# Optimization experiments

Measured on AMD Instinct MI355X. Metric: run time of the kernel, lower is better.

Reference implementation:

```python
import jax, jax.numpy as jnp
import numpy as np

NOTE_RES = 64  # global constant in the original repo; equals D of rep


def _down(x):
    # conv1d with kernel [0.5, 0.5], stride 2 over last axis (even length)
    return 0.5 * (x[..., ::2] + x[..., 1::2])


def setup_inputs() -> dict:
    key = jax.random.key(0)
    k1, k2, k3 = jax.random.split(key, 3)
    B, D, T = 32, NOTE_RES, 4096
    rep = jax.random.normal(k1, (B, D, T), dtype=jnp.float32)
    duration_mask = jax.random.uniform(k2, (B, D, T), dtype=jnp.float32)
    position_mask = jax.random.uniform(k3, (B, D, T), dtype=jnp.float32)
    return {
        "rep": rep,
        "duration_mask": duration_mask,
        "position_mask": position_mask,
        "low_duration": 1,
        "up_duration": 64,
    }


def reference(rep, duration_mask, position_mask, low_duration, up_duration):
    B, D, T = rep.shape  # D == NOTE_RES
    x = jnp.transpose(rep, (0, 2, 1))  # [B, T, NOTE_RES]; conv axis is last
    densed = _down(x)                  # [B, T, NOTE_RES//2]
    pot = NOTE_RES // 2
    res = jnp.zeros((B, T), dtype=rep.dtype)
    for i in range(0, NOTE_RES - low_duration):
        win_len = NOTE_RES - i - 1
        if win_len == pot:
            # descend one pyramid level
            x = densed
            densed = _down(x) if i < NOTE_RES - 2 else None
            d = x  # [B, T, win_len]
            pot //= 2
        else:
            pad_len = win_len - pot
            # mix fine-resolution prefix with coarse suffix -> length win_len
            d = jnp.concatenate([x[..., : 2 * pad_len], densed[..., pad_len:]], axis=-1)
        if win_len < up_duration:
            # sum_w d[b,t,w] * position_mask[b,w,t], gated by duration_mask[b,win_len-1,t]
            contrib = duration_mask[:, win_len - 1, :] * jnp.einsum(
                "btw,bwt->bt", d, position_mask[:, :win_len, :]
            )
            res = res + contrib
    return res[:, None, :]  # [B, 1, T]
```

## Files before the change

### kernel.cpp

```cpp
#include <hip/hip_runtime.h>


#define TT 4096

template <int M>
__device__ __forceinline__ void group_accum(const float* __restrict__ dmb,
                                            const float* pmv, const float* xa,
                                            const float* q, int low, int up,
                                            float& res) {
#pragma unroll
  for (int pad = 0, _dummy = 0; pad < M; ++pad) {
    (void)_dummy;
  }
  float p = 0.f;
#pragma unroll
  for (int pad = 0; pad < M; ++pad) {
    const int L = M + pad;
    float s = p;
#pragma unroll
    for (int k = pad; k < M; ++k) s = fmaf(xa[k], pmv[k + pad], s);
    if (L >= low && L < up)
      res = fmaf(dmb[(size_t)(M - 1 + pad) * TT], s, res);
    p += q[pad];
  }
}

template <int M>
__device__ __forceinline__ void downsample(const float* pmv, float* xa,
                                           float* q) {
#pragma unroll
  for (int j = 0; j < M; ++j) {
    const float a = xa[2 * j];
    const float c = xa[2 * j + 1];
    q[j] = a * pmv[2 * j] + c * pmv[2 * j + 1];
    xa[j] = 0.5f * (a + c);
  }
}

__global__ __launch_bounds__(256, 2) void ContextGenerator_34875134444049_kernel(
    const float* __restrict__ rep, const float* __restrict__ dm,
    const float* __restrict__ pm, const int* __restrict__ lowp,
    const int* __restrict__ upp, float* __restrict__ out, int n) {
  const int gid = blockIdx.x * 256 + threadIdx.x;
  if (gid >= n) return;
  const int t = gid & (TT - 1);
  const int b = gid >> 12;
  const size_t base = (size_t)b * 64 * TT + (size_t)t;

  const int low = lowp[0];
  const int up = upp[0];

  const float* __restrict__ repb = rep + base;
  const float* __restrict__ dmb = dm + base;
  const float* __restrict__ pmb = pm + base;

  float pmv[63];
#pragma unroll
  for (int w = 0; w < 63; ++w) pmv[w] = pmb[(size_t)w * TT];

  float xa[32];
  float q[32];
#pragma unroll
  for (int j = 0; j < 32; ++j) {
    const float a = repb[(size_t)(2 * j) * TT];
    const float c = repb[(size_t)(2 * j + 1) * TT];
    xa[j] = 0.5f * (a + c);
    q[j] = a * pmv[2 * j] + c * pmv[2 * j + 1];
  }

  float res = 0.f;
  group_accum<32>(dmb, pmv, xa, q, low, up, res);
  downsample<16>(pmv, xa, q);
  group_accum<16>(dmb, pmv, xa, q, low, up, res);
  downsample<8>(pmv, xa, q);
  group_accum<8>(dmb, pmv, xa, q, low, up, res);
  downsample<4>(pmv, xa, q);
  group_accum<4>(dmb, pmv, xa, q, low, up, res);
  downsample<2>(pmv, xa, q);
  group_accum<2>(dmb, pmv, xa, q, low, up, res);
  downsample<1>(pmv, xa, q);
  group_accum<1>(dmb, pmv, xa, q, low, up, res);

  out[gid] = res;
}

extern "C" void kernel_launch(void* const* d_in, const int* in_sizes, int n_in,
                              void* d_out, int out_size, void* d_ws,
                              size_t ws_size, hipStream_t stream) {
  const float* rep = (const float*)d_in[0];
  const float* dm = (const float*)d_in[1];
  const float* pm = (const float*)d_in[2];
  const int* lowp = (const int*)d_in[3];
  const int* upp = (const int*)d_in[4];
  float* out = (float*)d_out;

  const int n = out_size;
  const int blocks = (n + 255) / 256;
  ContextGenerator_34875134444049_kernel<<<blocks, 256, 0, stream>>>(
      rep, dm, pm, lowp, upp, out, n);
}
```

Before: 143.1 us.

## Split per-column work across four waves with LDS staging of rep and pm

Each block now handles 64 time columns. Its four waves cooperatively stage the rep and position_mask tiles into shared memory using asynchronous global-to-LDS loads. The window work is split into unequal roles: three waves cover slices of the first pyramid level and one wave covers the lower levels, and the four partial sums are reduced through LDS. This is meant to cut the per-thread register footprint, allowing four blocks per CU instead of two and raising parallelism and latency hiding. The costs are block synchronisations, extra LDS traffic, and possible load imbalance between the roles.

```diff
diff --git a/kernel.cpp b/kernel.cpp
--- a/kernel.cpp
+++ b/kernel.cpp
@@ -3,85 +3,156 @@
 
 #define TT 4096
 
+__device__ __forceinline__ void async_load_f32(const float* g, float* l) {
+  __builtin_amdgcn_global_load_lds(
+      (const __attribute__((address_space(1))) void*)g,
+      (__attribute__((address_space(3))) void*)l, 4, 0, 0);
+}
+
+template <int P0, int P1>
+__device__ __forceinline__ float role32(const float* __restrict__ lrep,
+                                        const float* __restrict__ lpm,
+                                        const float* dmr, int lane, int low,
+                                        int up) {
+  float xa[32 - P0];
+#pragma unroll
+  for (int k = P0; k < 32; ++k)
+    xa[k - P0] = 0.5f * (lrep[(2 * k) * 64 + lane] + lrep[(2 * k + 1) * 64 + lane]);
+  float q[P1 - 1];
+#pragma unroll
+  for (int j = 0; j < P1 - 1; ++j)
+    q[j] = lrep[(2 * j) * 64 + lane] * lpm[(2 * j) * 64 + lane] +
+           lrep[(2 * j + 1) * 64 + lane] * lpm[(2 * j + 1) * 64 + lane];
+  float p = 0.f;
+#pragma unroll
+  for (int j = 0; j < P0; ++j) p += q[j];
+  float res = 0.f;
+#pragma unroll
+  for (int pad = P0; pad < P1; ++pad) {
+    const int L = 32 + pad;
+    float s = p;
+#pragma unroll
+    for (int k = pad; k < 32; ++k)
+      s = fmaf(xa[k - P0], lpm[(k + pad) * 64 + lane], s);
+    if (L >= low && L < up) res = fmaf(dmr[pad - P0], s, res);
+    if (pad + 1 < P1) p += q[pad];
+  }
+  return res;
+}
+
 template <int M>
-__device__ __forceinline__ void group_accum(const float* __restrict__ dmb,
-                                            const float* pmv, const float* xa,
-                                            const float* q, int low, int up,
-                                            float& res) {
+__device__ __forceinline__ void down_lds(const float* __restrict__ lpm, int lane,
+                                         float* xa, float* q) {
 #pragma unroll
-  for (int pad = 0, _dummy = 0; pad < M; ++pad) {
-    (void)_dummy;
+  for (int j = 0; j < M; ++j) {
+    const float a = xa[2 * j];
+    const float c = xa[2 * j + 1];
+    q[j] = a * lpm[(2 * j) * 64 + lane] + c * lpm[(2 * j + 1) * 64 + lane];
+    xa[j] = 0.5f * (a + c);
   }
+}
+
+template <int M>
+__device__ __forceinline__ void acc_lds(const float* __restrict__ lpm,
+                                        const float* dmr, int lane,
+                                        const float* xa, const float* q, int low,
+                                        int up, float& res) {
   float p = 0.f;
 #pragma unroll
   for (int pad = 0; pad < M; ++pad) {
     const int L = M + pad;
     float s = p;
 #pragma unroll
-    for (int k = pad; k < M; ++k) s = fmaf(xa[k], pmv[k + pad], s);
-    if (L >= low && L < up)
-      res = fmaf(dmb[(size_t)(M - 1 + pad) * TT], s, res);
+    for (int k = pad; k < M; ++k) s = fmaf(xa[k], lpm[(k + pad) * 64 + lane], s);
+    if (L >= low && L < up) res = fmaf(dmr[M - 1 + pad], s, res);
     p += q[pad];
   }
 }
 
-template <int M>
-__device__ __forceinline__ void downsample(const float* pmv, float* xa,
-                                           float* q) {
+__device__ __forceinline__ float role_tail(const float* __restrict__ lrep,
+                                           const float* __restrict__ lpm,
+                                           const float* dmr, int lane, int low,
+                                           int up) {
+  float xa[32];
 #pragma unroll
-  for (int j = 0; j < M; ++j) {
-    const float a = xa[2 * j];
-    const float c = xa[2 * j + 1];
-    q[j] = a * pmv[2 * j] + c * pmv[2 * j + 1];
-    xa[j] = 0.5f * (a + c);
-  }
+  for (int k = 0; k < 32; ++k)
+    xa[k] = 0.5f * (lrep[(2 * k) * 64 + lane] + lrep[(2 * k + 1) * 64 + lane]);
+  float q[16];
+  float res = 0.f;
+  down_lds<16>(lpm, lane, xa, q);
+  acc_lds<16>(lpm, dmr, lane, xa, q, low, up, res);
+  down_lds<8>(lpm, lane, xa, q);
+  acc_lds<8>(lpm, dmr, lane, xa, q, low, up, res);
+  down_lds<4>(lpm, lane, xa, q);
+  acc_lds<4>(lpm, dmr, lane, xa, q, low, up, res);
+  down_lds<2>(lpm, lane, xa, q);
+  acc_lds<2>(lpm, dmr, lane, xa, q, low, up, res);
+  down_lds<1>(lpm, lane, xa, q);
+  acc_lds<1>(lpm, dmr, lane, xa, q, low, up, res);
+  return res;
 }
 
-__global__ __launch_bounds__(256, 2) void ContextGenerator_34875134444049_kernel(
+__global__ __launch_bounds__(256, 4) void ContextGenerator_34875134444049_kernel(
     const float* __restrict__ rep, const float* __restrict__ dm,
     const float* __restrict__ pm, const int* __restrict__ lowp,
-    const int* __restrict__ upp, float* __restrict__ out, int n) {
-  const int gid = blockIdx.x * 256 + threadIdx.x;
-  if (gid >= n) return;
-  const int t = gid & (TT - 1);
-  const int b = gid >> 12;
-  const size_t base = (size_t)b * 64 * TT + (size_t)t;
+    const int* __restrict__ upp, float* __restrict__ out) {
+  __shared__ float lds[128 * 64 + 4 * 64];
+  const int wid = threadIdx.x >> 6;
+  const int lane = threadIdx.x & 63;
+  const int b = blockIdx.x >> 6;
+  const int t0 = (blockIdx.x & 63) << 6;
+
+  const size_t base = (size_t)b * 64 * TT + (size_t)t0;
+
+  for (int r = wid; r < 127; r += 4) {
+    const float* src = (r < 64) ? rep + base + (size_t)r * TT
+                                : pm + base + (size_t)(r - 64) * TT;
+    async_load_f32(src + lane, &lds[r * 64]);
+  }
 
   const int low = lowp[0];
   const int up = upp[0];
 
-  const float* __restrict__ repb = rep + base;
-  const float* __restrict__ dmb = dm + base;
-  const float* __restrict__ pmb = pm + base;
-
-  float pmv[63];
+  const float* dmb = dm + base + lane;
+  float dmr[31];
+  if (wid == 0) {
 #pragma unroll
-  for (int w = 0; w < 63; ++w) pmv[w] = pmb[(size_t)w * TT];
-
-  float xa[32];
-  float q[32];
+    for (int i = 0; i < 6; ++i) dmr[i] = dmb[(size_t)(31 + i) * TT];
+  } else if (wid == 1) {
 #pragma unroll
-  for (int j = 0; j < 32; ++j) {
-    const float a = repb[(size_t)(2 * j) * TT];
-    const float c = repb[(size_t)(2 * j + 1) * TT];
-    xa[j] = 0.5f * (a + c);
-    q[j] = a * pmv[2 * j] + c * pmv[2 * j + 1];
+    for (int i = 0; i < 7; ++i) dmr[i] = dmb[(size_t)(37 + i) * TT];
+  } else if (wid == 2) {
+#pragma unroll
+    for (int i = 0; i < 19; ++i) dmr[i] = dmb[(size_t)(44 + i) * TT];
+  } else {
+#pragma unroll
+    for (int i = 0; i < 31; ++i) dmr[i] = dmb[(size_t)i * TT];
   }
 
-  float res = 0.f;
-  group_accum<32>(dmb, pmv, xa, q, low, up, res);
-  downsample<16>(pmv, xa, q);
-  group_accum<16>(dmb, pmv, xa, q, low, up, res);
-  downsample<8>(pmv, xa, q);
-  group_accum<8>(dmb, pmv, xa, q, low, up, res);
-  downsample<4>(pmv, xa, q);
-  group_accum<4>(dmb, pmv, xa, q, low, up, res);
-  downsample<2>(pmv, xa, q);
-  group_accum<2>(dmb, pmv, xa, q, low, up, res);
-  downsample<1>(pmv, xa, q);
-  group_accum<1>(dmb, pmv, xa, q, low, up, res);
+  __syncthreads();
 
-  out[gid] = res;
+  const float* lrep = lds;
+  const float* lpm = lds + 64 * 64;
+
+  float res;
+  if (wid == 0)
+    res = role32<0, 6>(lrep, lpm, dmr, lane, low, up);
+  else if (wid == 1)
+    res = role32<6, 13>(lrep, lpm, dmr, lane, low, up);
+  else if (wid == 2)
+    res = role32<13, 32>(lrep, lpm, dmr, lane, low, up);
+  else
+    res = role_tail(lrep, lpm, dmr, lane, low, up);
+
+  float* part = lds + 128 * 64;
+  part[wid * 64 + lane] = res;
+  __syncthreads();
+
+  if (threadIdx.x < 64) {
+    const float r = part[threadIdx.x] + part[64 + threadIdx.x] +
+                    part[128 + threadIdx.x] + part[192 + threadIdx.x];
+    out[(size_t)b * TT + t0 + threadIdx.x] = r;
+  }
 }
 
 extern "C" void kernel_launch(void* const* d_in, const int* in_sizes, int n_in,
@@ -94,8 +165,7 @@
   const int* upp = (const int*)d_in[4];
   float* out = (float*)d_out;
 
-  const int n = out_size;
-  const int blocks = (n + 255) / 256;
+  const int blocks = out_size / 64;
   ContextGenerator_34875134444049_kernel<<<blocks, 256, 0, stream>>>(
-      rep, dm, pm, lowp, upp, out, n);
+      rep, dm, pm, lowp, upp, out);
 }
```

Result: faster. 125.9 us (-12.0%).

## Split per-timestep work across two wavefronts and reduce via shared memory

Applied to the files above, without the earlier changes.

Each output column is now handled by two wavefronts: one computes the finest pyramid level (window lengths 32..63) and the other computes the prefix-sum terms plus all coarser levels, and the two partial sums are combined through shared memory. This halves the serial per-thread work and register pressure, which is meant to raise parallelism and occupancy (launch bounds change to 128 threads, 4 blocks). The trade-off is duplicated reads of rep and position_mask by both wavefronts, an added block barrier, and the loss of the bounds check on out_size.

```diff
diff --git a/kernel.cpp b/kernel.cpp
--- a/kernel.cpp
+++ b/kernel.cpp
@@ -3,85 +3,140 @@
 
 #define TT 4096
 
-template <int M>
-__device__ __forceinline__ void group_accum(const float* __restrict__ dmb,
-                                            const float* pmv, const float* xa,
-                                            const float* q, int low, int up,
-                                            float& res) {
-#pragma unroll
-  for (int pad = 0, _dummy = 0; pad < M; ++pad) {
-    (void)_dummy;
-  }
-  float p = 0.f;
-#pragma unroll
-  for (int pad = 0; pad < M; ++pad) {
-    const int L = M + pad;
-    float s = p;
-#pragma unroll
-    for (int k = pad; k < M; ++k) s = fmaf(xa[k], pmv[k + pad], s);
-    if (L >= low && L < up)
-      res = fmaf(dmb[(size_t)(M - 1 + pad) * TT], s, res);
-    p += q[pad];
-  }
-}
-
-template <int M>
-__device__ __forceinline__ void downsample(const float* pmv, float* xa,
-                                           float* q) {
-#pragma unroll
-  for (int j = 0; j < M; ++j) {
-    const float a = xa[2 * j];
-    const float c = xa[2 * j + 1];
-    q[j] = a * pmv[2 * j] + c * pmv[2 * j + 1];
-    xa[j] = 0.5f * (a + c);
-  }
-}
-
-__global__ __launch_bounds__(256, 2) void ContextGenerator_34875134444049_kernel(
+__global__ __launch_bounds__(128, 4) void ContextGenerator_34875134444049_kernel(
     const float* __restrict__ rep, const float* __restrict__ dm,
     const float* __restrict__ pm, const int* __restrict__ lowp,
-    const int* __restrict__ upp, float* __restrict__ out, int n) {
-  const int gid = blockIdx.x * 256 + threadIdx.x;
-  if (gid >= n) return;
-  const int t = gid & (TT - 1);
-  const int b = gid >> 12;
-  const size_t base = (size_t)b * 64 * TT + (size_t)t;
+    const int* __restrict__ upp, float* __restrict__ out) {
+  __shared__ float part[64];
+  const int wid = threadIdx.x >> 6;
+  const int lane = threadIdx.x & 63;
+  const int b = blockIdx.x >> 6;
+  const int t0 = (blockIdx.x & 63) << 6;
+  const size_t base = (size_t)b * 64 * TT + (size_t)t0 + (size_t)lane;
 
+  const float* __restrict__ repc = rep + base;
+  const float* __restrict__ pmc = pm + base;
+  const float* __restrict__ dmc = dm + base;
   const int low = lowp[0];
   const int up = upp[0];
 
-  const float* __restrict__ repb = rep + base;
-  const float* __restrict__ dmb = dm + base;
-  const float* __restrict__ pmb = pm + base;
+  float res = 0.f;
 
-  float pmv[63];
+  if (wid == 0) {
+    float pmv[63];
 #pragma unroll
-  for (int w = 0; w < 63; ++w) pmv[w] = pmb[(size_t)w * TT];
+    for (int r = 0; r < 63; ++r) pmv[r] = pmc[(size_t)r * TT];
+    float x1[32];
+#pragma unroll
+    for (int j = 0; j < 32; ++j)
+      x1[j] = 0.5f * (repc[(size_t)(2 * j) * TT] + repc[(size_t)(2 * j + 1) * TT]);
+#pragma unroll
+    for (int pad = 0; pad < 32; ++pad) {
+      const int L = 32 + pad;
+      float s = 0.f;
+#pragma unroll
+      for (int k = pad; k < 32; ++k) s = fmaf(x1[k], pmv[k + pad], s);
+      if (L >= low && L < up) res = fmaf(dmc[(size_t)(31 + pad) * TT], s, res);
+    }
+  } else {
+    float x1[32], pmv[32];
+    float P = 0.f;
+#pragma unroll
+    for (int j = 0; j < 31; ++j) {
+      const float a = repc[(size_t)(2 * j) * TT];
+      const float c = repc[(size_t)(2 * j + 1) * TT];
+      const float pa = pmc[(size_t)(2 * j) * TT];
+      const float pc = pmc[(size_t)(2 * j + 1) * TT];
+      x1[j] = 0.5f * (a + c);
+      if (2 * j < 32) pmv[2 * j] = pa;
+      if (2 * j + 1 < 32) pmv[2 * j + 1] = pc;
+      P = fmaf(a, pa, fmaf(c, pc, P));
+      const int L = 33 + j;
+      if (L >= low && L < up) res = fmaf(dmc[(size_t)(32 + j) * TT], P, res);
+    }
+    x1[31] = 0.5f * (repc[(size_t)62 * TT] + repc[(size_t)63 * TT]);
 
-  float xa[32];
-  float q[32];
+    float x2[16], q1[16];
 #pragma unroll
-  for (int j = 0; j < 32; ++j) {
-    const float a = repb[(size_t)(2 * j) * TT];
-    const float c = repb[(size_t)(2 * j + 1) * TT];
-    xa[j] = 0.5f * (a + c);
-    q[j] = a * pmv[2 * j] + c * pmv[2 * j + 1];
+    for (int j = 0; j < 16; ++j) {
+      x2[j] = 0.5f * (x1[2 * j] + x1[2 * j + 1]);
+      q1[j] = fmaf(x1[2 * j], pmv[2 * j], x1[2 * j + 1] * pmv[2 * j + 1]);
+    }
+    float p = 0.f;
+#pragma unroll
+    for (int pad = 0; pad < 16; ++pad) {
+      const int L = 16 + pad;
+      float s = p;
+#pragma unroll
+      for (int k = pad; k < 16; ++k) s = fmaf(x2[k], pmv[k + pad], s);
+      if (L >= low && L < up) res = fmaf(dmc[(size_t)(15 + pad) * TT], s, res);
+      p += q1[pad];
+    }
+
+    float x3[8], x4[4], x5[2];
+    {
+      float q[8];
+#pragma unroll
+      for (int j = 0; j < 8; ++j) {
+        x3[j] = 0.5f * (x2[2 * j] + x2[2 * j + 1]);
+        q[j] = fmaf(x2[2 * j], pmv[2 * j], x2[2 * j + 1] * pmv[2 * j + 1]);
+      }
+      float pp = 0.f;
+#pragma unroll
+      for (int pad = 0; pad < 8; ++pad) {
+        const int L = 8 + pad;
+        float s = pp;
+#pragma unroll
+        for (int k = pad; k < 8; ++k) s = fmaf(x3[k], pmv[k + pad], s);
+        if (L >= low && L < up) res = fmaf(dmc[(size_t)(7 + pad) * TT], s, res);
+        pp += q[pad];
+      }
+    }
+    {
+      float q[4];
+#pragma unroll
+      for (int j = 0; j < 4; ++j) {
+        x4[j] = 0.5f * (x3[2 * j] + x3[2 * j + 1]);
+        q[j] = fmaf(x3[2 * j], pmv[2 * j], x3[2 * j + 1] * pmv[2 * j + 1]);
+      }
+      float pp = 0.f;
+#pragma unroll
+      for (int pad = 0; pad < 4; ++pad) {
+        const int L = 4 + pad;
+        float s = pp;
+#pragma unroll
+        for (int k = pad; k < 4; ++k) s = fmaf(x4[k], pmv[k + pad], s);
+        if (L >= low && L < up) res = fmaf(dmc[(size_t)(3 + pad) * TT], s, res);
+        pp += q[pad];
+      }
+    }
+    {
+      float q[2];
+#pragma unroll
+      for (int j = 0; j < 2; ++j) {
+        x5[j] = 0.5f * (x4[2 * j] + x4[2 * j + 1]);
+        q[j] = fmaf(x4[2 * j], pmv[2 * j], x4[2 * j + 1] * pmv[2 * j + 1]);
+      }
+      float pp = 0.f;
+#pragma unroll
+      for (int pad = 0; pad < 2; ++pad) {
+        const int L = 2 + pad;
+        float s = pp;
+#pragma unroll
+        for (int k = pad; k < 2; ++k) s = fmaf(x5[k], pmv[k + pad], s);
+        if (L >= low && L < up) res = fmaf(dmc[(size_t)(1 + pad) * TT], s, res);
+        pp += q[pad];
+      }
+    }
+    {
+      const float x6 = 0.5f * (x5[0] + x5[1]);
+      if (1 >= low && 1 < up) res = fmaf(dmc[0], x6 * pmv[0], res);
+    }
   }
 
-  float res = 0.f;
-  group_accum<32>(dmb, pmv, xa, q, low, up, res);
-  downsample<16>(pmv, xa, q);
-  group_accum<16>(dmb, pmv, xa, q, low, up, res);
-  downsample<8>(pmv, xa, q);
-  group_accum<8>(dmb, pmv, xa, q, low, up, res);
-  downsample<4>(pmv, xa, q);
-  group_accum<4>(dmb, pmv, xa, q, low, up, res);
-  downsample<2>(pmv, xa, q);
-  group_accum<2>(dmb, pmv, xa, q, low, up, res);
-  downsample<1>(pmv, xa, q);
-  group_accum<1>(dmb, pmv, xa, q, low, up, res);
-
-  out[gid] = res;
+  if (wid == 1) part[lane] = res;
+  __syncthreads();
+  if (wid == 0) out[(size_t)b * TT + t0 + lane] = res + part[lane];
 }
 
 extern "C" void kernel_launch(void* const* d_in, const int* in_sizes, int n_in,
@@ -94,8 +149,7 @@
   const int* upp = (const int*)d_in[4];
   float* out = (float*)d_out;
 
-  const int n = out_size;
-  const int blocks = (n + 255) / 256;
-  ContextGenerator_34875134444049_kernel<<<blocks, 256, 0, stream>>>(
-      rep, dm, pm, lowp, upp, out, n);
+  const int blocks = out_size / 64;
+  ContextGenerator_34875134444049_kernel<<<blocks, 128, 0, stream>>>(
+      rep, dm, pm, lowp, upp, out);
 }
```

Result: slower. 158.3 us (+10.6%).
